# Kernel tuning notes

Measured on AMD Instinct MI355X. Metric: run time of the kernel, lower is better.

Reference implementation:

```python
import jax, jax.numpy as jnp
import numpy as np

NUM_HEADS = 4

def setup_inputs() -> dict:
    key = jax.random.key(0)
    ks = jax.random.split(key, 7)
    B, Lq, Lk, E, D, LAT = 16, 256, 4096, 64, 32, 32
    query = jax.random.normal(ks[0], (B, Lq, E), dtype=jnp.float32)
    key_in = jax.random.normal(ks[1], (B, Lk, E), dtype=jnp.float32)
    value = jax.random.normal(ks[2], (B, Lk, D), dtype=jnp.float32)
    mask = jax.random.randint(ks[3], (B, Lk, D), 0, 2, dtype=jnp.int32)
    Wq = jax.random.normal(ks[4], (E, E), dtype=jnp.float32) / np.sqrt(E).astype(np.float32)
    bq = jnp.zeros((E,), dtype=jnp.float32)
    Wk = jax.random.normal(ks[5], (E, E), dtype=jnp.float32) / np.sqrt(E).astype(np.float32)
    bk = jnp.zeros((E,), dtype=jnp.float32)
    Wo = jax.random.normal(ks[6], (NUM_HEADS * D, LAT), dtype=jnp.float32) / np.sqrt(NUM_HEADS * D).astype(np.float32)
    bo = jnp.zeros((LAT,), dtype=jnp.float32)
    return {"query": query, "key": key_in, "value": value, "mask": mask,
            "Wq": Wq, "bq": bq, "Wk": Wk, "bk": bk, "Wo": Wo, "bo": bo}

def reference(query, key, value, mask, Wq, bq, Wk, bk, Wo, bo):
    B, Lk, D = value.shape
    Lq = query.shape[1]
    h = NUM_HEADS
    ek = query.shape[-1] // h  # embed_time_k
    # linear maps (torch Linear: y = x @ W; here W stored as (in, out))
    q = (query @ Wq + bq).reshape(B, Lq, h, ek).transpose(0, 2, 1, 3)  # (B,h,Lq,ek)
    k = (key @ Wk + bk).reshape(B, Lk, h, ek).transpose(0, 2, 1, 3)    # (B,h,Lk,ek)
    scores = jnp.einsum('bhqe,bhke->bhqk', q, k) / jnp.sqrt(jnp.asarray(ek, q.dtype))
    # Original repeats scores over D, masks per-feature with -inf, softmaxes over Lk,
    # then does a weighted sum. Equivalent fused form (never builds (B,h,Lq,Lk,D)):
    e = jnp.exp(scores - jnp.max(scores, axis=-1, keepdims=True))  # (B,h,Lq,Lk)
    m = mask.astype(value.dtype)                                   # (B,Lk,D) 0/1
    num = jnp.einsum('bhqk,bkd->bhqd', e, m * value)
    den = jnp.einsum('bhqk,bkd->bhqd', e, m)
    x = num / den                                                  # (B,h,Lq,D)
    x = x.transpose(0, 2, 1, 3).reshape(B, Lq, h * D)
    return x @ Wo + bo  # (B, Lq, latent_dim)
```

## Files before the change

kernel.cpp:

```cpp
#include <hip/hip_runtime.h>
#include <hip/hip_bf16.h>
#include <math.h>

typedef __bf16 bf16;
typedef bf16 bf16x4 __attribute__((ext_vector_type(4)));
typedef bf16 bf16x8 __attribute__((ext_vector_type(8)));
typedef float f32x4 __attribute__((ext_vector_type(4)));
typedef float f32x16 __attribute__((ext_vector_type(16)));

#define B_   16
#define LQ_  256
#define LK_  4096
#define E_   64
#define H_   4
#define EK_  16
#define D_   32
#define LAT_ 32

#define OFF_QP    0u
#define OFF_KP    524288u
#define OFF_MVFB  8912896u
#define OFF_WOT   17301504u
#define OFF_NDP   17309696u
#define WS_NEED   50864128u

#define LOG2E 1.44269504f

__device__ inline f32x4 mfma_bf16(bf16x8 a, bf16x8 b, f32x4 c) {
  return __builtin_amdgcn_mfma_f32_16x16x32_bf16(a, b, c, 0, 0, 0);
}
__device__ inline f32x16 mfma_bf16_32(bf16x8 a, bf16x8 b, f32x16 c) {
  return __builtin_amdgcn_mfma_f32_32x32x16_bf16(a, b, c, 0, 0, 0);
}

__global__ __launch_bounds__(256) void prep_kernel(
    const float* __restrict__ query, const float* __restrict__ key,
    const float* __restrict__ value, const int* __restrict__ mask,
    const float* __restrict__ Wq, const float* __restrict__ bq,
    const float* __restrict__ Wk, const float* __restrict__ bk,
    const float* __restrict__ Wo,
    bf16* __restrict__ qp, bf16* __restrict__ kp,
    bf16* __restrict__ mvfB, bf16* __restrict__ WoT)
{
  __shared__ __align__(16) bf16 s_b[16896];
  const int bid = blockIdx.x;
  const int tid = threadIdx.x;

  if (bid < 544) {
    const bool isQ = bid < 32;
    const int row0 = isQ ? bid * 128 : (bid - 32) * 128;
    const float* in   = isQ ? query : key;
    const float* W    = isQ ? Wq : Wk;
    const float* bias = isQ ? bq : bk;
    bf16* outp        = isQ ? qp : kp;
    const float scal  = isQ ? (0.25f * LOG2E) : 1.0f;

    bf16* sIn = s_b;
    bf16* sWT = s_b + 9216;

#pragma unroll
    for (int p = 0; p < 8; ++p) {
      int f4 = tid + p * 256;
      int row = f4 >> 4, e4 = (f4 & 15) * 4;
      float4 v = *(const float4*)(in + (size_t)(row0 + row) * 64 + e4);
      bf16x4 b4;
      b4[0] = (bf16)v.x; b4[1] = (bf16)v.y; b4[2] = (bf16)v.z; b4[3] = (bf16)v.w;
      *(bf16x4*)(sIn + row * 72 + e4) = b4;
    }
#pragma unroll
    for (int p = 0; p < 4; ++p) {
      int f4 = tid + p * 256;
      int k = f4 >> 4, c4 = (f4 & 15) * 4;
      float4 v = *(const float4*)(W + k * 64 + c4);
      sWT[(c4 + 0) * 72 + k] = (bf16)v.x;
      sWT[(c4 + 1) * 72 + k] = (bf16)v.y;
      sWT[(c4 + 2) * 72 + k] = (bf16)v.z;
      sWT[(c4 + 3) * 72 + k] = (bf16)v.w;
    }
    __syncthreads();

    const int w = tid >> 6, l = tid & 63, l15 = l & 15, g = l >> 4;
    f32x4 acc[2][4];
#pragma unroll
    for (int mt = 0; mt < 2; ++mt)
#pragma unroll
      for (int nt = 0; nt < 4; ++nt) acc[mt][nt] = f32x4{0.f, 0.f, 0.f, 0.f};

#pragma unroll
    for (int ks = 0; ks < 2; ++ks) {
      bf16x8 A0 = *(bf16x8*)(sIn + (32 * w + l15) * 72 + 32 * ks + 8 * g);
      bf16x8 A1 = *(bf16x8*)(sIn + (32 * w + 16 + l15) * 72 + 32 * ks + 8 * g);
#pragma unroll
      for (int nt = 0; nt < 4; ++nt) {
        bf16x8 Bf = *(bf16x8*)(sWT + (16 * nt + l15) * 72 + 32 * ks + 8 * g);
        acc[0][nt] = mfma_bf16(A0, Bf, acc[0][nt]);
        acc[1][nt] = mfma_bf16(A1, Bf, acc[1][nt]);
      }
    }
#pragma unroll
    for (int mt = 0; mt < 2; ++mt)
#pragma unroll
      for (int nt = 0; nt < 4; ++nt) {
        int col = 16 * nt + l15;
        float bv = bias[col];
#pragma unroll
        for (int r = 0; r < 4; ++r) {
          int row = row0 + 32 * w + 16 * mt + 4 * g + r;
          outp[(size_t)row * 64 + col] = (bf16)((acc[mt][nt][r] + bv) * scal);
        }
      }
  } else if (bid < 800) {
    const int rb = bid - 544;
    const int b = rb >> 4, kk0 = (rb & 15) * 256;
#pragma unroll
    for (int p = 0; p < 8; ++p) {
      int f4 = tid + p * 256;
      int kk = f4 >> 3, d4 = (f4 & 7) * 4;
      size_t gi = ((size_t)(b * LK_ + kk0 + kk)) * 32 + d4;
      float4 v = *(const float4*)(value + gi);
      int4   m = *(const int4*)(mask + gi);
      s_b[(d4 + 0) * 264 + kk] = (bf16)(m.x ? v.x : 0.0f);
      s_b[(d4 + 1) * 264 + kk] = (bf16)(m.y ? v.y : 0.0f);
      s_b[(d4 + 2) * 264 + kk] = (bf16)(m.z ? v.z : 0.0f);
      s_b[(d4 + 3) * 264 + kk] = (bf16)(m.w ? v.w : 0.0f);
      s_b[(32 + d4 + 0) * 264 + kk] = (bf16)(float)m.x;
      s_b[(32 + d4 + 1) * 264 + kk] = (bf16)(float)m.y;
      s_b[(32 + d4 + 2) * 264 + kk] = (bf16)(float)m.z;
      s_b[(32 + d4 + 3) * 264 + kk] = (bf16)(float)m.w;
    }
    __syncthreads();
    const int col = tid >> 2, seg = tid & 3;
    const int nt = col >> 4, l15c = col & 15;
#pragma unroll
    for (int w2 = 0; w2 < 8; ++w2) {
      int kkg = seg * 64 + w2 * 8;
      int tile = (kk0 + kkg) >> 5;
      int gq = (kkg >> 3) & 3;
      int lane = 16 * gq + l15c;
      uint4 d = *(uint4*)(s_b + col * 264 + kkg);
      *(uint4*)(mvfB + (size_t)((((b * 128 + tile) * 4 + nt) * 64 + lane)) * 8) = d;
    }
  } else {
#pragma unroll
    for (int p = 0; p < 16; ++p) {
      int f = tid + p * 256;
      int k = f >> 5, n = f & 31;
      WoT[n * 128 + k] = (bf16)Wo[f];
    }
  }
}

__global__ __launch_bounds__(256, 4) void attn_kernel(
    const bf16* __restrict__ qp, const bf16* __restrict__ kp,
    const bf16* __restrict__ mvfB, float* __restrict__ ndp)
{
  __shared__ __align__(16) bf16 s_se[4 * 1280];

  const int bid = blockIdx.x;
  const int kc = bid & 7, qt = (bid >> 3) & 7, b = bid >> 6;
  const int tid = threadIdx.x;
  const int h = tid >> 6, l = tid & 63, l15 = l & 15, g = l >> 4;
  const int l31 = l & 31, hi = l >> 5;
  const int q0 = qt * 32;
  const int tile0 = kc * 16;

  bf16x8 qB = *(const bf16x8*)(qp + (size_t)((b * LQ_ + q0 + l31) * 64 + h * EK_ + hi * 8));

  f32x4 acc[2][4];
#pragma unroll
  for (int mt = 0; mt < 2; ++mt)
#pragma unroll
    for (int nt = 0; nt < 4; ++nt) acc[mt][nt] = f32x4{0.f, 0.f, 0.f, 0.f};

  bf16* se_w = s_se + h * 1280;
  const bf16* mvt0 = mvfB + (size_t)(b * 128 + tile0) * 2048;
  const bf16* kp_b = kp + (size_t)(b * LK_ + tile0 * 32) * 64 + h * EK_ + hi * 8;

#pragma unroll 2
  for (int t = 0; t < 16; ++t) {
    const bf16* mvt = mvt0 + (size_t)t * 2048;

    bf16x8 mvB[4];
#pragma unroll
    for (int nt = 0; nt < 4; ++nt)
      mvB[nt] = *(const bf16x8*)(mvt + (nt * 64 + l) * 8);

    bf16x8 kA = *(const bf16x8*)(kp_b + (size_t)(t * 32 + l31) * 64);

    f32x16 S;
#pragma unroll
    for (int i = 0; i < 16; ++i) S[i] = 0.f;
    S = mfma_bf16_32(kA, qB, S);

#pragma unroll
    for (int rq = 0; rq < 4; ++rq) {
      bf16x4 e4;
#pragma unroll
      for (int r = 0; r < 4; ++r) e4[r] = (bf16)exp2f(S[4 * rq + r]);
      *(bf16x4*)(se_w + l31 * 40 + 8 * rq + 4 * hi) = e4;
    }

    asm volatile("" ::: "memory");

#pragma unroll
    for (int mq = 0; mq < 2; ++mq) {
      bf16x8 eA = *(bf16x8*)(se_w + (16 * mq + l15) * 40 + 8 * g);
#pragma unroll
      for (int nt = 0; nt < 4; ++nt)
        acc[mq][nt] = mfma_bf16(eA, mvB[nt], acc[mq][nt]);
    }
  }

  float* ndp_w = ndp + ((((size_t)kc * B_ + b) * H_ + h) * LQ_) * 64;
#pragma unroll
  for (int mt = 0; mt < 2; ++mt)
#pragma unroll
    for (int nt = 0; nt < 4; ++nt)
#pragma unroll
      for (int r = 0; r < 4; ++r) {
        int q = q0 + 16 * mt + 4 * g + r;
        int col = 16 * nt + l15;
        ndp_w[(size_t)q * 64 + col] = acc[mt][nt][r];
      }
}

__global__ __launch_bounds__(256) void out_kernel(
    const float* __restrict__ ndp, const bf16* __restrict__ WoT,
    const float* __restrict__ bo, float* __restrict__ out)
{
  __shared__ __align__(16) bf16 s_x[16 * 136];
  const int bid = blockIdx.x;
  const int b = bid >> 4, q0 = (bid & 15) * 16;
  const int tid = threadIdx.x;
  const int q = tid >> 4, jg = tid & 15;
  const int h = jg >> 2, d0 = (jg & 3) * 8;

  f32x4 nlo = f32x4{0.f,0.f,0.f,0.f}, nhi = f32x4{0.f,0.f,0.f,0.f};
  f32x4 dlo = f32x4{0.f,0.f,0.f,0.f}, dhi = f32x4{0.f,0.f,0.f,0.f};
#pragma unroll
  for (int kc = 0; kc < 8; ++kc) {
    const float* p = ndp + ((((size_t)kc * B_ + b) * H_ + h) * LQ_ + q0 + q) * 64;
    nlo += *(const f32x4*)(p + d0);
    nhi += *(const f32x4*)(p + d0 + 4);
    dlo += *(const f32x4*)(p + 32 + d0);
    dhi += *(const f32x4*)(p + 32 + d0 + 4);
  }
  bf16* sx = s_x + q * 136 + h * 32 + d0;
#pragma unroll
  for (int i = 0; i < 4; ++i) {
    sx[i]     = (bf16)(nlo[i] / dlo[i]);
    sx[4 + i] = (bf16)(nhi[i] / dhi[i]);
  }
  __syncthreads();
  const int w = tid >> 6, l = tid & 63, l15 = l & 15, g = l >> 4;
  if (w < 2) {
    const int nt = w;
    f32x4 acc = f32x4{0.f, 0.f, 0.f, 0.f};
#pragma unroll
    for (int ks = 0; ks < 4; ++ks) {
      bf16x8 A  = *(bf16x8*)(s_x + l15 * 136 + 32 * ks + 8 * g);
      bf16x8 Bf = *(const bf16x8*)(WoT + (l15 + 16 * nt) * 128 + 32 * ks + 8 * g);
      acc = mfma_bf16(A, Bf, acc);
    }
    float bv = bo[l15 + 16 * nt];
#pragma unroll
    for (int r = 0; r < 4; ++r) {
      int row = q0 + 4 * g + r;
      out[(size_t)(b * LQ_ + row) * LAT_ + l15 + 16 * nt] = acc[r] + bv;
    }
  }
}

extern "C" void kernel_launch(void* const* d_in, const int* in_sizes, int n_in,
                              void* d_out, int out_size, void* d_ws, size_t ws_size,
                              hipStream_t stream) {
  const float* query = (const float*)d_in[0];
  const float* key   = (const float*)d_in[1];
  const float* value = (const float*)d_in[2];
  const int*   mask  = (const int*)d_in[3];
  const float* Wq    = (const float*)d_in[4];
  const float* bq    = (const float*)d_in[5];
  const float* Wk    = (const float*)d_in[6];
  const float* bk    = (const float*)d_in[7];
  const float* Wo    = (const float*)d_in[8];
  const float* bo    = (const float*)d_in[9];
  float* out = (float*)d_out;
  char* ws = (char*)d_ws;

  if (ws_size < (size_t)WS_NEED) return;

  bf16* qp   = (bf16*)(ws + OFF_QP);
  bf16* kp   = (bf16*)(ws + OFF_KP);
  bf16* mvfB = (bf16*)(ws + OFF_MVFB);
  bf16* WoT  = (bf16*)(ws + OFF_WOT);
  float* ndp = (float*)(ws + OFF_NDP);

  prep_kernel<<<801, 256, 0, stream>>>(query, key, value, mask, Wq, bq, Wk, bk,
                                       Wo, qp, kp, mvfB, WoT);
  attn_kernel<<<1024, 256, 0, stream>>>(qp, kp, mvfB, ndp);
  out_kernel<<<256, 256, 0, stream>>>(ndp, WoT, bo, out);
}
```

Before: 125.4 us.

## Keep softmax probabilities in registers via permlane32 swap, use 32x32 MFMA for PV

```diff
diff --git a/kernel.cpp b/kernel.cpp
--- a/kernel.cpp
+++ b/kernel.cpp
@@ -3,10 +3,13 @@
 #include <math.h>
 
 typedef __bf16 bf16;
+typedef bf16 bf16x2 __attribute__((ext_vector_type(2)));
 typedef bf16 bf16x4 __attribute__((ext_vector_type(4)));
 typedef bf16 bf16x8 __attribute__((ext_vector_type(8)));
 typedef float f32x4 __attribute__((ext_vector_type(4)));
 typedef float f32x16 __attribute__((ext_vector_type(16)));
+typedef unsigned int u32x2 __attribute__((ext_vector_type(2)));
+typedef unsigned int u32x4 __attribute__((ext_vector_type(4)));
 
 #define B_   16
 #define LQ_  256
@@ -31,6 +34,15 @@
 }
 __device__ inline f32x16 mfma_bf16_32(bf16x8 a, bf16x8 b, f32x16 c) {
   return __builtin_amdgcn_mfma_f32_32x32x16_bf16(a, b, c, 0, 0, 0);
+}
+
+__device__ inline void pl32swap(unsigned &a, unsigned &b) {
+#if __has_builtin(__builtin_amdgcn_permlane32_swap)
+  u32x2 r = __builtin_amdgcn_permlane32_swap(a, b, false, false);
+  a = r[0]; b = r[1];
+#else
+  asm volatile("v_permlane32_swap_b32 %0, %1" : "+v"(a), "+v"(b));
+#endif
 }
 
 __global__ __launch_bounds__(256) void prep_kernel(
@@ -130,15 +142,16 @@
     }
     __syncthreads();
     const int col = tid >> 2, seg = tid & 3;
-    const int nt = col >> 4, l15c = col & 15;
+    const int nd = col >> 5, n31 = col & 31;
 #pragma unroll
     for (int w2 = 0; w2 < 8; ++w2) {
       int kkg = seg * 64 + w2 * 8;
       int tile = (kk0 + kkg) >> 5;
-      int gq = (kkg >> 3) & 3;
-      int lane = 16 * gq + l15c;
+      int ks   = (kkg >> 4) & 1;
+      int hi2  = (kkg >> 3) & 1;
+      int lane = n31 + 32 * hi2;
       uint4 d = *(uint4*)(s_b + col * 264 + kkg);
-      *(uint4*)(mvfB + (size_t)((((b * 128 + tile) * 4 + nt) * 64 + lane)) * 8) = d;
+      *(uint4*)(mvfB + (size_t)((((b * 128 + tile) * 2 + ks) * 2 + nd) * 64 + lane) * 8) = d;
     }
   } else {
 #pragma unroll
@@ -154,25 +167,20 @@
     const bf16* __restrict__ qp, const bf16* __restrict__ kp,
     const bf16* __restrict__ mvfB, float* __restrict__ ndp)
 {
-  __shared__ __align__(16) bf16 s_se[4 * 1280];
-
   const int bid = blockIdx.x;
   const int kc = bid & 7, qt = (bid >> 3) & 7, b = bid >> 6;
   const int tid = threadIdx.x;
-  const int h = tid >> 6, l = tid & 63, l15 = l & 15, g = l >> 4;
+  const int h = tid >> 6, l = tid & 63;
   const int l31 = l & 31, hi = l >> 5;
   const int q0 = qt * 32;
   const int tile0 = kc * 16;
 
   bf16x8 qB = *(const bf16x8*)(qp + (size_t)((b * LQ_ + q0 + l31) * 64 + h * EK_ + hi * 8));
 
-  f32x4 acc[2][4];
-#pragma unroll
-  for (int mt = 0; mt < 2; ++mt)
-#pragma unroll
-    for (int nt = 0; nt < 4; ++nt) acc[mt][nt] = f32x4{0.f, 0.f, 0.f, 0.f};
-
-  bf16* se_w = s_se + h * 1280;
+  f32x16 accN, accD, Z;
+#pragma unroll
+  for (int i = 0; i < 16; ++i) { accN[i] = 0.f; accD[i] = 0.f; Z[i] = 0.f; }
+
   const bf16* mvt0 = mvfB + (size_t)(b * 128 + tile0) * 2048;
   const bf16* kp_b = kp + (size_t)(b * LK_ + tile0 * 32) * 64 + h * EK_ + hi * 8;
 
@@ -180,48 +188,44 @@
   for (int t = 0; t < 16; ++t) {
     const bf16* mvt = mvt0 + (size_t)t * 2048;
 
-    bf16x8 mvB[4];
-#pragma unroll
-    for (int nt = 0; nt < 4; ++nt)
-      mvB[nt] = *(const bf16x8*)(mvt + (nt * 64 + l) * 8);
+    bf16x8 Bn0 = *(const bf16x8*)(mvt + (0 * 64 + l) * 8);
+    bf16x8 Bd0 = *(const bf16x8*)(mvt + (1 * 64 + l) * 8);
+    bf16x8 Bn1 = *(const bf16x8*)(mvt + (2 * 64 + l) * 8);
+    bf16x8 Bd1 = *(const bf16x8*)(mvt + (3 * 64 + l) * 8);
 
     bf16x8 kA = *(const bf16x8*)(kp_b + (size_t)(t * 32 + l31) * 64);
 
-    f32x16 S;
-#pragma unroll
-    for (int i = 0; i < 16; ++i) S[i] = 0.f;
-    S = mfma_bf16_32(kA, qB, S);
-
-#pragma unroll
-    for (int rq = 0; rq < 4; ++rq) {
-      bf16x4 e4;
-#pragma unroll
-      for (int r = 0; r < 4; ++r) e4[r] = (bf16)exp2f(S[4 * rq + r]);
-      *(bf16x4*)(se_w + l31 * 40 + 8 * rq + 4 * hi) = e4;
-    }
-
-    asm volatile("" ::: "memory");
-
-#pragma unroll
-    for (int mq = 0; mq < 2; ++mq) {
-      bf16x8 eA = *(bf16x8*)(se_w + (16 * mq + l15) * 40 + 8 * g);
-#pragma unroll
-      for (int nt = 0; nt < 4; ++nt)
-        acc[mq][nt] = mfma_bf16(eA, mvB[nt], acc[mq][nt]);
-    }
-  }
-
-  float* ndp_w = ndp + ((((size_t)kc * B_ + b) * H_ + h) * LQ_) * 64;
-#pragma unroll
-  for (int mt = 0; mt < 2; ++mt)
-#pragma unroll
-    for (int nt = 0; nt < 4; ++nt)
-#pragma unroll
-      for (int r = 0; r < 4; ++r) {
-        int q = q0 + 16 * mt + 4 * g + r;
-        int col = 16 * nt + l15;
-        ndp_w[(size_t)q * 64 + col] = acc[mt][nt][r];
-      }
+    f32x16 S = mfma_bf16_32(kA, qB, Z);
+
+    unsigned P[8];
+#pragma unroll
+    for (int i = 0; i < 8; ++i) {
+      union { bf16x2 hh; unsigned u; } cv;
+      cv.hh[0] = (bf16)exp2f(S[2 * i + 0]);
+      cv.hh[1] = (bf16)exp2f(S[2 * i + 1]);
+      P[i] = cv.u;
+    }
+    pl32swap(P[0], P[2]);
+    pl32swap(P[1], P[3]);
+    pl32swap(P[4], P[6]);
+    pl32swap(P[5], P[7]);
+    union { u32x4 u; bf16x8 v; } pa0, pa1;
+    pa0.u = (u32x4){P[0], P[1], P[2], P[3]};
+    pa1.u = (u32x4){P[4], P[5], P[6], P[7]};
+
+    accN = mfma_bf16_32(pa0.v, Bn0, accN);
+    accD = mfma_bf16_32(pa0.v, Bd0, accD);
+    accN = mfma_bf16_32(pa1.v, Bn1, accN);
+    accD = mfma_bf16_32(pa1.v, Bd1, accD);
+  }
+
+  float* ndp_w = ndp + ((((size_t)kc * B_ + b) * H_ + h) * LQ_ + q0) * 64;
+#pragma unroll
+  for (int r = 0; r < 16; ++r) {
+    int q = (r & 3) + 8 * (r >> 2) + 4 * hi;
+    ndp_w[(size_t)q * 64 + l31]      = accN[r];
+    ndp_w[(size_t)q * 64 + 32 + l31] = accD[r];
+  }
 }
 
 __global__ __launch_bounds__(256) void out_kernel(
```

Measured after the change: 125.9 us. Within noise of the previous version (+0.3%).
